# Kernel optimization log

Hardware: AMD Instinct MI355X
Metric: run time of the kernel (lower is better)

The kernel has to match this reference:

```python
import jax, jax.numpy as jnp
import numpy as np


def setup_inputs() -> dict:
    key = jax.random.key(0)
    k1, k2, k3 = jax.random.split(key, 3)
    p = 4096
    target = jax.random.normal(k1, (p, p), dtype=jnp.float32)
    source = jax.random.normal(k2, (p, p), dtype=jnp.float32)
    W_beta = jax.random.uniform(k3, (p, p), dtype=jnp.float32)
    return {"target": target, "source": source, "W_beta": W_beta}


def reference(target, source, W_beta):
    # X = target, Y = source (module-level names in the original).
    # denominator inner loop: sum_i X[i] . X[i] == ||X||_F^2 (scalar),
    # recomputed p^2 times in the original; computed once here.
    s = jnp.sum(target * target)
    W = W_beta.sum(axis=1)                       # [p]
    W2 = W * W                                   # [p]
    scale = W2 / (s * W2 + 1.0)                  # [p]
    G = jnp.matmul(source, target.T)             # [p,p], G[i,j] = Y[i] . X[j]
    W_matrix = scale[:, None] * G                # [p,p]
    primary = jnp.matmul(W_matrix, target) - source
    loss = jnp.sqrt(jnp.sum(jnp.square(jnp.matmul(W_beta, primary))))
    return loss, W_matrix
```

## Files before the change

### kernel.cpp

```cpp
#include <hip/hip_runtime.h>
#include <hip/hip_bf16.h>

#define PDIM 4096
#define PPN ((size_t)PDIM * (size_t)PDIM)

typedef __attribute__((ext_vector_type(8))) short bf16x8;
typedef __attribute__((ext_vector_type(4))) float floatx4;
typedef __attribute__((ext_vector_type(8))) int int8v;

__device__ __forceinline__ void load_lds16(const void* g, void* l) {
  __builtin_amdgcn_global_load_lds(
      (const __attribute__((address_space(1))) void*)g,
      (__attribute__((address_space(3))) void*)l, 16, 0, 0);
}

__device__ __forceinline__ unsigned short bf16bits(float f) {
  __hip_bfloat16 h = __float2bfloat16(f);
  return *(unsigned short*)&h;
}

__device__ __forceinline__ unsigned char fp8byte(float v) {
  return (unsigned char)(__builtin_amdgcn_cvt_pk_fp8_f32(v, v, 0, false) & 0xff);
}
__device__ __forceinline__ unsigned int fp8x4(float a, float b, float c, float d) {
  int v = __builtin_amdgcn_cvt_pk_fp8_f32(a, b, 0, false);
  v = __builtin_amdgcn_cvt_pk_fp8_f32(c, d, v, true);
  return (unsigned int)v;
}

__global__ void sumsq(const float4* __restrict__ x, float* __restrict__ acc) {
  float s = 0.f;
  const size_t n4 = PPN / 4;
  for (size_t i = (size_t)blockIdx.x * 256 + threadIdx.x; i < n4;
       i += (size_t)gridDim.x * 256) {
    const float4 v = x[i];
    s += v.x * v.x + v.y * v.y + v.z * v.z + v.w * v.w;
  }
#pragma unroll
  for (int off = 32; off > 0; off >>= 1) s += __shfl_down(s, off);
  __shared__ float ws[4];
  if ((threadIdx.x & 63) == 0) ws[threadIdx.x >> 6] = s;
  __syncthreads();
  if (threadIdx.x == 0) atomicAdd(acc, ws[0] + ws[1] + ws[2] + ws[3]);
}

__global__ void cast_x(const float* __restrict__ src,
                       __hip_bfloat16* __restrict__ dstN,
                       unsigned char* __restrict__ dstT8) {
  __shared__ float tile[64][65];
  const int bx = blockIdx.x * 64, by = blockIdx.y * 64;
  const int tx = threadIdx.x & 15, ty = threadIdx.x >> 4;
#pragma unroll
  for (int r = 0; r < 4; ++r) {
    const int row = ty + r * 16;
    const float4 v = *(const float4*)&src[(size_t)(by + row) * PDIM + bx + tx * 4];
    tile[row][tx * 4 + 0] = v.x;
    tile[row][tx * 4 + 1] = v.y;
    tile[row][tx * 4 + 2] = v.z;
    tile[row][tx * 4 + 3] = v.w;
    ushort4 o;
    o.x = bf16bits(v.x); o.y = bf16bits(v.y); o.z = bf16bits(v.z); o.w = bf16bits(v.w);
    *(ushort4*)&dstN[(size_t)(by + row) * PDIM + bx + tx * 4] = o;
  }
  __syncthreads();
#pragma unroll
  for (int r = 0; r < 4; ++r) {
    const int i = ty + r * 16;
    *(unsigned int*)&dstT8[(size_t)(bx + i) * PDIM + by + tx * 4] =
        fp8x4(tile[tx * 4 + 0][i], tile[tx * 4 + 1][i],
              tile[tx * 4 + 2][i], tile[tx * 4 + 3][i]);
  }
}

__global__ void cast_y(const float* __restrict__ src,
                       __hip_bfloat16* __restrict__ dstN,
                       __hip_bfloat16* __restrict__ dstT) {
  __shared__ float tile[64][65];
  const int bx = blockIdx.x * 64, by = blockIdx.y * 64;
  const int tx = threadIdx.x & 15, ty = threadIdx.x >> 4;
#pragma unroll
  for (int r = 0; r < 4; ++r) {
    const int row = ty + r * 16;
    const float4 v = *(const float4*)&src[(size_t)(by + row) * PDIM + bx + tx * 4];
    tile[row][tx * 4 + 0] = v.x;
    tile[row][tx * 4 + 1] = v.y;
    tile[row][tx * 4 + 2] = v.z;
    tile[row][tx * 4 + 3] = v.w;
    ushort4 o;
    o.x = bf16bits(v.x); o.y = bf16bits(v.y); o.z = bf16bits(v.z); o.w = bf16bits(v.w);
    *(ushort4*)&dstN[(size_t)(by + row) * PDIM + bx + tx * 4] = o;
  }
  __syncthreads();
#pragma unroll
  for (int r = 0; r < 4; ++r) {
    const int i = ty + r * 16;
    ushort4 o;
    o.x = bf16bits(tile[tx * 4 + 0][i]);
    o.y = bf16bits(tile[tx * 4 + 1][i]);
    o.z = bf16bits(tile[tx * 4 + 2][i]);
    o.w = bf16bits(tile[tx * 4 + 3][i]);
    *(ushort4*)&dstT[(size_t)(bx + i) * PDIM + by + tx * 4] = o;
  }
}

__global__ void cast_wb_rows(const float* __restrict__ Wb,
                             unsigned char* __restrict__ Wb8,
                             const float* __restrict__ sAcc,
                             float* __restrict__ scale) {
  const size_t row = blockIdx.x;
  const float4* src = (const float4*)(Wb + row * PDIM);
  unsigned int* dst = (unsigned int*)(Wb8 + row * PDIM);
  float sum = 0.f;
#pragma unroll
  for (int it = 0; it < 4; ++it) {
    const int j = threadIdx.x + it * 256;
    const float4 v = src[j];
    sum += (v.x + v.y) + (v.z + v.w);
    dst[j] = fp8x4(v.x, v.y, v.z, v.w);
  }
#pragma unroll
  for (int off = 32; off > 0; off >>= 1) sum += __shfl_down(sum, off);
  __shared__ float ws[4];
  if ((threadIdx.x & 63) == 0) ws[threadIdx.x >> 6] = sum;
  __syncthreads();
  if (threadIdx.x == 0) {
    const float W = ws[0] + ws[1] + ws[2] + ws[3];
    const float w2 = W * W;
    scale[row] = w2 / ((*sAcc) * w2 + 1.0f);
  }
}

__device__ __forceinline__ void mfma_quad(floatx4 (&acc)[8][4], int mo, int no,
                                          const bf16x8 (&af)[8],
                                          const bf16x8 (&bf)[4]) {
  __builtin_amdgcn_s_setprio(1);
#pragma unroll
  for (int mi = 0; mi < 4; ++mi)
#pragma unroll
    for (int ni = 0; ni < 2; ++ni)
#pragma unroll
      for (int kk = 0; kk < 2; ++kk)
        acc[mo + mi][no + ni] = __builtin_amdgcn_mfma_f32_16x16x32_bf16(
            af[mi * 2 + kk], bf[ni * 2 + kk], acc[mo + mi][no + ni], 0, 0, 0);
  __builtin_amdgcn_s_setprio(0);
}

__device__ __forceinline__ void read_a(bf16x8 (&dst)[8], const char* base, int slot0) {
#pragma unroll
  for (int mi = 0; mi < 4; ++mi) {
    dst[mi * 2 + 0] = *(const bf16x8*)(base + mi * 2048 + slot0);
    dst[mi * 2 + 1] = *(const bf16x8*)(base + mi * 2048 + (slot0 ^ 64));
  }
}
__device__ __forceinline__ void read_b(bf16x8 (&dst)[4], const char* base, int slot0) {
#pragma unroll
  for (int ni = 0; ni < 2; ++ni) {
    dst[ni * 2 + 0] = *(const bf16x8*)(base + ni * 2048 + slot0);
    dst[ni * 2 + 1] = *(const bf16x8*)(base + ni * 2048 + (slot0 ^ 64));
  }
}

__global__ __launch_bounds__(512, 2)
void gemm_bf16_wm(const __hip_bfloat16* __restrict__ A,
                  const __hip_bfloat16* __restrict__ B,
                  const float* __restrict__ scale,
                  float* __restrict__ outF,
                  unsigned char* __restrict__ Wm8) {
  __shared__ __align__(16) char LDS[131072];

  const int tid = threadIdx.x;
  const int lane = tid & 63;
  const int wave = tid >> 6;
  const int wm = wave >> 2;
  const int wn = wave & 3;

  const int bid = blockIdx.x;
  const int swz = (bid & 7) * 32 + (bid >> 3);
  const int bx = swz & 15;
  const int by = swz >> 4;
  const size_t rowA0 = (size_t)by * 256;
  const size_t rowB0 = (size_t)bx * 256;

  const int srow = tid >> 3;
  const int scol = ((tid & 7) ^ (srow & 7)) << 4;
  const char* pA = (const char*)A + (rowA0 + srow) * 8192 + scol;
  const char* pB = (const char*)B + (rowB0 + srow) * 8192 + scol;
  const int ldsWav = wave * 1024;

  const int fr = lane & 15;
  const int kq = lane >> 4;
  const int slot0 = ((kq ^ (fr & 7)) << 4);
  const int aRowB = (wm * 64 + fr) * 128;
  const int bRowB = (wn * 32 + fr) * 128;

  floatx4 acc[8][4] = {};
  bf16x8 afLo[8], afHi[8], bLo[4], bHi[4];

  {
    char* dA0 = LDS + ldsWav;
    char* dB0 = LDS + 65536 + ldsWav;
    load_lds16(pA, dA0);                         load_lds16(pA + 524288, dA0 + 8192);
    load_lds16(pB, dB0);                         load_lds16(pB + 524288, dB0 + 8192);
    load_lds16(pB + 1048576, dB0 + 16384);       load_lds16(pB + 1572864, dB0 + 24576);
    load_lds16(pA + 1048576, dA0 + 16384);       load_lds16(pA + 1572864, dA0 + 24576);
    char* dA1 = dA0 + 32768;
    char* dB1 = dB0 + 32768;
    load_lds16(pA + 128, dA1);                   load_lds16(pA + 128 + 524288, dA1 + 8192);
    load_lds16(pB + 128, dB1);                   load_lds16(pB + 128 + 524288, dB1 + 8192);
    load_lds16(pB + 128 + 1048576, dB1 + 16384); load_lds16(pB + 128 + 1572864, dB1 + 24576);
    load_lds16(pA + 128 + 1048576, dA1 + 16384); load_lds16(pA + 128 + 1572864, dA1 + 24576);
  }
  asm volatile("s_waitcnt vmcnt(8)" ::: "memory");
  __builtin_amdgcn_s_barrier();
  read_a(afLo, (const char*)LDS + aRowB, slot0);
  read_b(bLo, (const char*)LDS + 65536 + bRowB, slot0);
  asm volatile("s_waitcnt lgkmcnt(0)" ::: "memory");
  __builtin_amdgcn_s_barrier();

  for (int t = 0; t < 64; ++t) {
    const int buf = (t & 1) << 15;
    const int tS = (t + 2) & 63;
    const char* sA = pA + (size_t)tS * 128;
    const char* sB = pB + (size_t)tS * 128;
    char* dA = LDS + buf + ldsWav;
    char* dB = LDS + 65536 + buf + ldsWav;
    const char* aRd  = LDS + buf + aRowB;
    const char* bRd  = LDS + 65536 + buf + bRowB;
    const char* aRdN = LDS + (buf ^ 32768) + aRowB;
    const char* bRdN = LDS + 65536 + (buf ^ 32768) + bRowB;

    load_lds16(sA, dA);
    load_lds16(sA + 524288, dA + 8192);
    mfma_quad(acc, 0, 0, afLo, bLo);
    read_b(bHi, bRd + 16384, slot0);
    __builtin_amdgcn_s_barrier();

    load_lds16(sB, dB);
    load_lds16(sB + 524288, dB + 8192);
    mfma_quad(acc, 0, 2, afLo, bHi);
    read_a(afHi, aRd + 16384, slot0);
    __builtin_amdgcn_s_barrier();

    asm volatile("s_waitcnt vmcnt(10)" ::: "memory");
    load_lds16(sB + 1048576, dB + 16384);
    load_lds16(sB + 1572864, dB + 24576);
    mfma_quad(acc, 4, 2, afHi, bHi);
    read_a(afLo, aRdN, slot0);
    __builtin_amdgcn_s_barrier();

    asm volatile("s_waitcnt vmcnt(6)" ::: "memory");
    load_lds16(sA + 1048576, dA + 16384);
    load_lds16(sA + 1572864, dA + 24576);
    mfma_quad(acc, 4, 0, afHi, bLo);
    read_b(bLo, bRdN, slot0);
    __builtin_amdgcn_s_barrier();
  }

  const int lr = (lane >> 4) << 2;
  const int lc = lane & 15;
#pragma unroll
  for (int mi = 0; mi < 8; ++mi) {
    const size_t rbase = rowA0 + (size_t)(mi >> 2) * 128 + wm * 64 + (mi & 3) * 16 + lr;
#pragma unroll
    for (int r = 0; r < 4; ++r) {
      const size_t row = rbase + r;
      const float sc = scale[row];
#pragma unroll
      for (int ni = 0; ni < 4; ++ni) {
        const size_t col = rowB0 + (size_t)(ni >> 1) * 128 + wn * 32 + (ni & 1) * 16 + lc;
        const float v = sc * acc[mi][ni][r];
        outF[row * PDIM + col] = v;
        Wm8[row * PDIM + col] = fp8byte(v * 131072.f);
      }
    }
  }
}

union f8frag { int8v v; int4 h[2]; };

__device__ __forceinline__ void mfma_quad8(floatx4 (&acc)[8][4], int mo, int no,
                                           const f8frag (&af)[4],
                                           const f8frag (&bf)[2]) {
  __builtin_amdgcn_s_setprio(1);
#pragma unroll
  for (int mi = 0; mi < 4; ++mi)
#pragma unroll
    for (int ni = 0; ni < 2; ++ni)
      acc[mo + mi][no + ni] = __builtin_amdgcn_mfma_scale_f32_16x16x128_f8f6f4(
          af[mi].v, bf[ni].v, acc[mo + mi][no + ni],
          0 , 0 , 0, 0x7F7F7F7F, 0, 0x7F7F7F7F);
  __builtin_amdgcn_s_setprio(0);
}

__device__ __forceinline__ void read_a8(f8frag (&dst)[4], const char* base,
                                        int offLo, int offHi) {
#pragma unroll
  for (int mi = 0; mi < 4; ++mi) {
    dst[mi].h[0] = *(const int4*)(base + mi * 2048 + offLo);
    dst[mi].h[1] = *(const int4*)(base + mi * 2048 + offHi);
  }
}
__device__ __forceinline__ void read_b8(f8frag (&dst)[2], const char* base,
                                        int offLo, int offHi) {
#pragma unroll
  for (int ni = 0; ni < 2; ++ni) {
    dst[ni].h[0] = *(const int4*)(base + ni * 2048 + offLo);
    dst[ni].h[1] = *(const int4*)(base + ni * 2048 + offHi);
  }
}

template <int MODE>
__global__ __launch_bounds__(512, 2)
void gemm_fp8(const unsigned char* __restrict__ A,
              const unsigned char* __restrict__ B,
              const __hip_bfloat16* __restrict__ sub,
              unsigned char* __restrict__ outP,
              float* __restrict__ lossAcc) {
  __shared__ __align__(16) char LDS[131072];

  const int tid = threadIdx.x;
  const int lane = tid & 63;
  const int wave = tid >> 6;
  const int wm = wave >> 2;
  const int wn = wave & 3;

  const int bid = blockIdx.x;
  const int swz = (bid & 7) * 32 + (bid >> 3);
  const int bx = swz & 15;
  const int by = swz >> 4;
  const size_t rowA0 = (size_t)by * 256;
  const size_t rowB0 = (size_t)bx * 256;

  const int srow = tid >> 3;
  const int scol = ((tid & 7) ^ (srow & 7)) << 4;
  const char* pA = (const char*)A + (rowA0 + srow) * 4096 + scol;
  const char* pB = (const char*)B + (rowB0 + srow) * 4096 + scol;
  const int ldsWav = wave * 1024;

  const int fr = lane & 15;
  const int e = fr & 7;
  const int q2 = (lane >> 4) << 1;
  const int offLo = (q2 ^ e) << 4;
  const int offHi = ((q2 + 1) ^ e) << 4;
  const int aRowB = (wm * 64 + fr) * 128;
  const int bRowB = (wn * 32 + fr) * 128;

  floatx4 acc[8][4] = {};
  f8frag afLo[4], afHi[4], bLo[2], bHi[2];

  {
    char* dA0 = LDS + ldsWav;
    char* dB0 = LDS + 65536 + ldsWav;
    load_lds16(pA, dA0);                        load_lds16(pA + 262144, dA0 + 8192);
    load_lds16(pB, dB0);                        load_lds16(pB + 262144, dB0 + 8192);
    load_lds16(pB + 524288, dB0 + 16384);       load_lds16(pB + 786432, dB0 + 24576);
    load_lds16(pA + 524288, dA0 + 16384);       load_lds16(pA + 786432, dA0 + 24576);
    char* dA1 = dA0 + 32768;
    char* dB1 = dB0 + 32768;
    load_lds16(pA + 128, dA1);                  load_lds16(pA + 128 + 262144, dA1 + 8192);
    load_lds16(pB + 128, dB1);                  load_lds16(pB + 128 + 262144, dB1 + 8192);
    load_lds16(pB + 128 + 524288, dB1 + 16384); load_lds16(pB + 128 + 786432, dB1 + 24576);
    load_lds16(pA + 128 + 524288, dA1 + 16384); load_lds16(pA + 128 + 786432, dA1 + 24576);
  }
  asm volatile("s_waitcnt vmcnt(8)" ::: "memory");
  __builtin_amdgcn_s_barrier();
  read_a8(afLo, (const char*)LDS + aRowB, offLo, offHi);
  read_b8(bLo, (const char*)LDS + 65536 + bRowB, offLo, offHi);
  asm volatile("s_waitcnt lgkmcnt(0)" ::: "memory");
  __builtin_amdgcn_s_barrier();

  for (int t = 0; t < 32; ++t) {
    const int buf = (t & 1) << 15;
    const int tS = (t + 2) & 31;
    const char* sA = pA + (size_t)tS * 128;
    const char* sB = pB + (size_t)tS * 128;
    char* dA = LDS + buf + ldsWav;
    char* dB = LDS + 65536 + buf + ldsWav;
    const char* aRd  = LDS + buf + aRowB;
    const char* bRd  = LDS + 65536 + buf + bRowB;
    const char* aRdN = LDS + (buf ^ 32768) + aRowB;
    const char* bRdN = LDS + 65536 + (buf ^ 32768) + bRowB;

    load_lds16(sA, dA);
    load_lds16(sA + 262144, dA + 8192);
    mfma_quad8(acc, 0, 0, afLo, bLo);
    read_b8(bHi, bRd + 16384, offLo, offHi);
    __builtin_amdgcn_s_barrier();

    load_lds16(sB, dB);
    load_lds16(sB + 262144, dB + 8192);
    mfma_quad8(acc, 0, 2, afLo, bHi);
    read_a8(afHi, aRd + 16384, offLo, offHi);
    __builtin_amdgcn_s_barrier();

    asm volatile("s_waitcnt vmcnt(10)" ::: "memory");
    load_lds16(sB + 524288, dB + 16384);
    load_lds16(sB + 786432, dB + 24576);
    mfma_quad8(acc, 4, 2, afHi, bHi);
    read_a8(afLo, aRdN, offLo, offHi);
    __builtin_amdgcn_s_barrier();

    asm volatile("s_waitcnt vmcnt(6)" ::: "memory");
    load_lds16(sA + 524288, dA + 16384);
    load_lds16(sA + 786432, dA + 24576);
    mfma_quad8(acc, 4, 0, afHi, bLo);
    read_b8(bLo, bRdN, offLo, offHi);
    __builtin_amdgcn_s_barrier();
  }

  const int lr = (lane >> 4) << 2;
  const int lc = lane & 15;

  if constexpr (MODE == 2) {
    float tot = 0.f;
#pragma unroll
    for (int mi = 0; mi < 8; ++mi)
#pragma unroll
      for (int ni = 0; ni < 4; ++ni)
#pragma unroll
        for (int r = 0; r < 4; ++r) tot += acc[mi][ni][r] * acc[mi][ni][r];
#pragma unroll
    for (int off = 32; off > 0; off >>= 1) tot += __shfl_down(tot, off);
    __shared__ float ws[8];
    if (lane == 0) ws[wave] = tot;
    __syncthreads();
    if (tid == 0)
      atomicAdd(lossAcc, ws[0] + ws[1] + ws[2] + ws[3] + ws[4] + ws[5] + ws[6] + ws[7]);
  } else {
    constexpr float INV = 1.f / 131072.f;
#pragma unroll
    for (int mi = 0; mi < 8; ++mi) {
      const size_t rbase = rowA0 + (size_t)(mi >> 2) * 128 + wm * 64 + (mi & 3) * 16 + lr;
#pragma unroll
      for (int r = 0; r < 4; ++r) {
        const size_t row = rbase + r;
#pragma unroll
        for (int ni = 0; ni < 4; ++ni) {
          const size_t col = rowB0 + (size_t)(ni >> 1) * 128 + wn * 32 + (ni & 1) * 16 + lc;
          const float v = acc[mi][ni][r] * INV - __bfloat162float(sub[row * PDIM + col]);
          outP[row * PDIM + col] = fp8byte(v);
        }
      }
    }
  }
}

__global__ void finalize(float* __restrict__ out, const float* __restrict__ acc) {
  if (threadIdx.x == 0) out[0] = sqrtf(*acc);
}

extern "C" void kernel_launch(void* const* d_in, const int* in_sizes, int n_in,
                              void* d_out, int out_size, void* d_ws, size_t ws_size,
                              hipStream_t stream) {
  const float* X  = (const float*)d_in[0];
  const float* Y  = (const float*)d_in[1];
  const float* Wb = (const float*)d_in[2];
  float* out = (float*)d_out;

  __hip_bfloat16* Xb   = (__hip_bfloat16*)d_ws;
  __hip_bfloat16* Yb   = Xb + PPN;
  __hip_bfloat16* YbT  = Yb + PPN;
  unsigned char*  XT8  = (unsigned char*)(YbT + PPN);
  unsigned char*  Wm8  = XT8 + PPN;
  unsigned char*  Wb8  = Wm8 + PPN;
  unsigned char*  PT8  = Wb8 + PPN;
  float* scale   = (float*)(PT8 + PPN);
  float* sAcc    = scale + PDIM;
  float* lossAcc = sAcc + 1;

  hipMemsetAsync(sAcc, 0, 2 * sizeof(float), stream);

  sumsq<<<1024, 256, 0, stream>>>((const float4*)X, sAcc);

  dim3 cgrid(PDIM / 64, PDIM / 64);
  cast_x<<<cgrid, 256, 0, stream>>>(X, Xb, XT8);
  cast_y<<<cgrid, 256, 0, stream>>>(Y, Yb, YbT);
  cast_wb_rows<<<PDIM, 256, 0, stream>>>(Wb, Wb8, sAcc, scale);

  gemm_bf16_wm<<<dim3(256), 512, 0, stream>>>(Yb, Xb, scale, out + 1, Wm8);

  gemm_fp8<1><<<dim3(256), 512, 0, stream>>>(XT8, Wm8, YbT, PT8, nullptr);
  gemm_fp8<2><<<dim3(256), 512, 0, stream>>>(PT8, Wb8, nullptr, nullptr, lossAcc);

  finalize<<<1, 1, 0, stream>>>(out, lossAcc);
}
```

Baseline: 520.6 us.

## Fuse sum-of-squares into cast_x and load FP8 GEMM fragments directly from global

The separate sumsq reduction kernel is removed. The Frobenius sum of squares is now accumulated inside cast_x, which already reads X, so one full pass over the input and one launch disappear. The FP8 GEMM no longer stages tiles through LDS with async global-to-LDS copies and barriers. Each wave instead loads its MFMA fragments straight from global memory, prefetching one quarter-step ahead. This drops LDS traffic and barriers, but it gives up sharing data between waves through LDS and exposes global memory latency to the MFMA chain, relying on caches for reuse.

```diff
diff --git a/kernel.cpp b/kernel.cpp
--- a/kernel.cpp
+++ b/kernel.cpp
@@ -28,32 +28,20 @@
   return (unsigned int)v;
 }
 
-__global__ void sumsq(const float4* __restrict__ x, float* __restrict__ acc) {
-  float s = 0.f;
-  const size_t n4 = PPN / 4;
-  for (size_t i = (size_t)blockIdx.x * 256 + threadIdx.x; i < n4;
-       i += (size_t)gridDim.x * 256) {
-    const float4 v = x[i];
-    s += v.x * v.x + v.y * v.y + v.z * v.z + v.w * v.w;
-  }
-#pragma unroll
-  for (int off = 32; off > 0; off >>= 1) s += __shfl_down(s, off);
-  __shared__ float ws[4];
-  if ((threadIdx.x & 63) == 0) ws[threadIdx.x >> 6] = s;
-  __syncthreads();
-  if (threadIdx.x == 0) atomicAdd(acc, ws[0] + ws[1] + ws[2] + ws[3]);
-}
-
 __global__ void cast_x(const float* __restrict__ src,
                        __hip_bfloat16* __restrict__ dstN,
-                       unsigned char* __restrict__ dstT8) {
+                       unsigned char* __restrict__ dstT8,
+                       float* __restrict__ sAcc) {
   __shared__ float tile[64][65];
+  __shared__ float ws[4];
   const int bx = blockIdx.x * 64, by = blockIdx.y * 64;
   const int tx = threadIdx.x & 15, ty = threadIdx.x >> 4;
+  float s = 0.f;
 #pragma unroll
   for (int r = 0; r < 4; ++r) {
     const int row = ty + r * 16;
     const float4 v = *(const float4*)&src[(size_t)(by + row) * PDIM + bx + tx * 4];
+    s += v.x * v.x + v.y * v.y + v.z * v.z + v.w * v.w;
     tile[row][tx * 4 + 0] = v.x;
     tile[row][tx * 4 + 1] = v.y;
     tile[row][tx * 4 + 2] = v.z;
@@ -62,6 +50,9 @@
     o.x = bf16bits(v.x); o.y = bf16bits(v.y); o.z = bf16bits(v.z); o.w = bf16bits(v.w);
     *(ushort4*)&dstN[(size_t)(by + row) * PDIM + bx + tx * 4] = o;
   }
+#pragma unroll
+  for (int off = 32; off > 0; off >>= 1) s += __shfl_down(s, off);
+  if ((threadIdx.x & 63) == 0) ws[threadIdx.x >> 6] = s;
   __syncthreads();
 #pragma unroll
   for (int r = 0; r < 4; ++r) {
@@ -70,6 +61,7 @@
         fp8x4(tile[tx * 4 + 0][i], tile[tx * 4 + 1][i],
               tile[tx * 4 + 2][i], tile[tx * 4 + 3][i]);
   }
+  if (threadIdx.x == 0) atomicAdd(sAcc, ws[0] + ws[1] + ws[2] + ws[3]);
 }
 
 __global__ void cast_y(const float* __restrict__ src,
@@ -292,20 +284,20 @@
   __builtin_amdgcn_s_setprio(0);
 }
 
-__device__ __forceinline__ void read_a8(f8frag (&dst)[4], const char* base,
-                                        int offLo, int offHi) {
+__device__ __forceinline__ void gread_a8(f8frag (&dst)[4],
+                                         const unsigned char* base) {
 #pragma unroll
   for (int mi = 0; mi < 4; ++mi) {
-    dst[mi].h[0] = *(const int4*)(base + mi * 2048 + offLo);
-    dst[mi].h[1] = *(const int4*)(base + mi * 2048 + offHi);
-  }
-}
-__device__ __forceinline__ void read_b8(f8frag (&dst)[2], const char* base,
-                                        int offLo, int offHi) {
+    dst[mi].h[0] = *(const int4*)(base + (size_t)mi * 65536);
+    dst[mi].h[1] = *(const int4*)(base + (size_t)mi * 65536 + 16);
+  }
+}
+__device__ __forceinline__ void gread_b8(f8frag (&dst)[2],
+                                         const unsigned char* base) {
 #pragma unroll
   for (int ni = 0; ni < 2; ++ni) {
-    dst[ni].h[0] = *(const int4*)(base + ni * 2048 + offLo);
-    dst[ni].h[1] = *(const int4*)(base + ni * 2048 + offHi);
+    dst[ni].h[0] = *(const int4*)(base + (size_t)ni * 65536);
+    dst[ni].h[1] = *(const int4*)(base + (size_t)ni * 65536 + 16);
   }
 }
 
@@ -316,8 +308,6 @@
               const __hip_bfloat16* __restrict__ sub,
               unsigned char* __restrict__ outP,
               float* __restrict__ lossAcc) {
-  __shared__ __align__(16) char LDS[131072];
-
   const int tid = threadIdx.x;
   const int lane = tid & 63;
   const int wave = tid >> 6;
@@ -331,81 +321,33 @@
   const size_t rowA0 = (size_t)by * 256;
   const size_t rowB0 = (size_t)bx * 256;
 
-  const int srow = tid >> 3;
-  const int scol = ((tid & 7) ^ (srow & 7)) << 4;
-  const char* pA = (const char*)A + (rowA0 + srow) * 4096 + scol;
-  const char* pB = (const char*)B + (rowB0 + srow) * 4096 + scol;
-  const int ldsWav = wave * 1024;
-
   const int fr = lane & 15;
-  const int e = fr & 7;
   const int q2 = (lane >> 4) << 1;
-  const int offLo = (q2 ^ e) << 4;
-  const int offHi = ((q2 + 1) ^ e) << 4;
-  const int aRowB = (wm * 64 + fr) * 128;
-  const int bRowB = (wn * 32 + fr) * 128;
+
+  const unsigned char* pAlo = A + (rowA0 + wm * 64 + fr) * (size_t)PDIM + q2 * 16;
+  const unsigned char* pAhi = pAlo + (size_t)128 * PDIM;
+  const unsigned char* pBlo = B + (rowB0 + wn * 32 + fr) * (size_t)PDIM + q2 * 16;
+  const unsigned char* pBhi = pBlo + (size_t)128 * PDIM;
 
   floatx4 acc[8][4] = {};
   f8frag afLo[4], afHi[4], bLo[2], bHi[2];
 
-  {
-    char* dA0 = LDS + ldsWav;
-    char* dB0 = LDS + 65536 + ldsWav;
-    load_lds16(pA, dA0);                        load_lds16(pA + 262144, dA0 + 8192);
-    load_lds16(pB, dB0);                        load_lds16(pB + 262144, dB0 + 8192);
-    load_lds16(pB + 524288, dB0 + 16384);       load_lds16(pB + 786432, dB0 + 24576);
-    load_lds16(pA + 524288, dA0 + 16384);       load_lds16(pA + 786432, dA0 + 24576);
-    char* dA1 = dA0 + 32768;
-    char* dB1 = dB0 + 32768;
-    load_lds16(pA + 128, dA1);                  load_lds16(pA + 128 + 262144, dA1 + 8192);
-    load_lds16(pB + 128, dB1);                  load_lds16(pB + 128 + 262144, dB1 + 8192);
-    load_lds16(pB + 128 + 524288, dB1 + 16384); load_lds16(pB + 128 + 786432, dB1 + 24576);
-    load_lds16(pA + 128 + 524288, dA1 + 16384); load_lds16(pA + 128 + 786432, dA1 + 24576);
-  }
-  asm volatile("s_waitcnt vmcnt(8)" ::: "memory");
-  __builtin_amdgcn_s_barrier();
-  read_a8(afLo, (const char*)LDS + aRowB, offLo, offHi);
-  read_b8(bLo, (const char*)LDS + 65536 + bRowB, offLo, offHi);
-  asm volatile("s_waitcnt lgkmcnt(0)" ::: "memory");
-  __builtin_amdgcn_s_barrier();
+  gread_a8(afLo, pAlo);
+  gread_b8(bLo, pBlo);
 
   for (int t = 0; t < 32; ++t) {
-    const int buf = (t & 1) << 15;
-    const int tS = (t + 2) & 31;
-    const char* sA = pA + (size_t)tS * 128;
-    const char* sB = pB + (size_t)tS * 128;
-    char* dA = LDS + buf + ldsWav;
-    char* dB = LDS + 65536 + buf + ldsWav;
-    const char* aRd  = LDS + buf + aRowB;
-    const char* bRd  = LDS + 65536 + buf + bRowB;
-    const char* aRdN = LDS + (buf ^ 32768) + aRowB;
-    const char* bRdN = LDS + 65536 + (buf ^ 32768) + bRowB;
-
-    load_lds16(sA, dA);
-    load_lds16(sA + 262144, dA + 8192);
+    const size_t kt = (size_t)t * 128;
+
     mfma_quad8(acc, 0, 0, afLo, bLo);
-    read_b8(bHi, bRd + 16384, offLo, offHi);
-    __builtin_amdgcn_s_barrier();
-
-    load_lds16(sB, dB);
-    load_lds16(sB + 262144, dB + 8192);
+    gread_b8(bHi, pBhi + kt);
+
     mfma_quad8(acc, 0, 2, afLo, bHi);
-    read_a8(afHi, aRd + 16384, offLo, offHi);
-    __builtin_amdgcn_s_barrier();
-
-    asm volatile("s_waitcnt vmcnt(10)" ::: "memory");
-    load_lds16(sB + 524288, dB + 16384);
-    load_lds16(sB + 786432, dB + 24576);
+    gread_a8(afHi, pAhi + kt);
+
     mfma_quad8(acc, 4, 2, afHi, bHi);
-    read_a8(afLo, aRdN, offLo, offHi);
-    __builtin_amdgcn_s_barrier();
-
-    asm volatile("s_waitcnt vmcnt(6)" ::: "memory");
-    load_lds16(sA + 524288, dA + 16384);
-    load_lds16(sA + 786432, dA + 24576);
+    gread_a8(afLo, pAlo + kt + 128);
     mfma_quad8(acc, 4, 0, afHi, bLo);
-    read_b8(bLo, bRdN, offLo, offHi);
-    __builtin_amdgcn_s_barrier();
+    gread_b8(bLo, pBlo + kt + 128);
   }
 
   const int lr = (lane >> 4) << 2;
@@ -470,10 +412,8 @@
 
   hipMemsetAsync(sAcc, 0, 2 * sizeof(float), stream);
 
-  sumsq<<<1024, 256, 0, stream>>>((const float4*)X, sAcc);
-
   dim3 cgrid(PDIM / 64, PDIM / 64);
-  cast_x<<<cgrid, 256, 0, stream>>>(X, Xb, XT8);
+  cast_x<<<cgrid, 256, 0, stream>>>(X, Xb, XT8, sAcc);
   cast_y<<<cgrid, 256, 0, stream>>>(Y, Yb, YbT);
   cast_wb_rows<<<PDIM, 256, 0, stream>>>(Wb, Wb8, sAcc, scale);
 
```

New measurement: 719.5 us. +38.2%, slower.

## Fuse Frobenius sum-of-squares into cast_x and restructure bf16 GEMM LDS pipeline

Applied to the files above, without the earlier changes.

Removes the separate sumsq kernel by accumulating the squared sum of X inside cast_x, reduced per block and added with one atomic, which avoids a second full read of X and one launch. It also reworks the main loop of the bf16 GEMM: LDS fragment reads are no longer prefetched from the other buffer during the previous step. Each step now reads its own fragments, waits on lgkmcnt, and has extra barriers between the MFMA quads. This lengthens the dependency between LDS reads and MFMAs and may reduce overlap, and the vmcnt(10) wait is dropped, so global-to-LDS ordering depends on the remaining vmcnt(6).

```diff
diff --git a/kernel.cpp b/kernel.cpp
--- a/kernel.cpp
+++ b/kernel.cpp
@@ -28,32 +28,20 @@
   return (unsigned int)v;
 }
 
-__global__ void sumsq(const float4* __restrict__ x, float* __restrict__ acc) {
-  float s = 0.f;
-  const size_t n4 = PPN / 4;
-  for (size_t i = (size_t)blockIdx.x * 256 + threadIdx.x; i < n4;
-       i += (size_t)gridDim.x * 256) {
-    const float4 v = x[i];
-    s += v.x * v.x + v.y * v.y + v.z * v.z + v.w * v.w;
-  }
-#pragma unroll
-  for (int off = 32; off > 0; off >>= 1) s += __shfl_down(s, off);
-  __shared__ float ws[4];
-  if ((threadIdx.x & 63) == 0) ws[threadIdx.x >> 6] = s;
-  __syncthreads();
-  if (threadIdx.x == 0) atomicAdd(acc, ws[0] + ws[1] + ws[2] + ws[3]);
-}
-
 __global__ void cast_x(const float* __restrict__ src,
                        __hip_bfloat16* __restrict__ dstN,
-                       unsigned char* __restrict__ dstT8) {
+                       unsigned char* __restrict__ dstT8,
+                       float* __restrict__ sAcc) {
   __shared__ float tile[64][65];
+  __shared__ float ws[4];
   const int bx = blockIdx.x * 64, by = blockIdx.y * 64;
   const int tx = threadIdx.x & 15, ty = threadIdx.x >> 4;
+  float s = 0.f;
 #pragma unroll
   for (int r = 0; r < 4; ++r) {
     const int row = ty + r * 16;
     const float4 v = *(const float4*)&src[(size_t)(by + row) * PDIM + bx + tx * 4];
+    s += v.x * v.x + v.y * v.y + v.z * v.z + v.w * v.w;
     tile[row][tx * 4 + 0] = v.x;
     tile[row][tx * 4 + 1] = v.y;
     tile[row][tx * 4 + 2] = v.z;
@@ -62,6 +50,9 @@
     o.x = bf16bits(v.x); o.y = bf16bits(v.y); o.z = bf16bits(v.z); o.w = bf16bits(v.w);
     *(ushort4*)&dstN[(size_t)(by + row) * PDIM + bx + tx * 4] = o;
   }
+#pragma unroll
+  for (int off = 32; off > 0; off >>= 1) s += __shfl_down(s, off);
+  if ((threadIdx.x & 63) == 0) ws[threadIdx.x >> 6] = s;
   __syncthreads();
 #pragma unroll
   for (int r = 0; r < 4; ++r) {
@@ -70,6 +61,7 @@
         fp8x4(tile[tx * 4 + 0][i], tile[tx * 4 + 1][i],
               tile[tx * 4 + 2][i], tile[tx * 4 + 3][i]);
   }
+  if (threadIdx.x == 0) atomicAdd(sAcc, ws[0] + ws[1] + ws[2] + ws[3]);
 }
 
 __global__ void cast_y(const float* __restrict__ src,
@@ -212,10 +204,6 @@
   }
   asm volatile("s_waitcnt vmcnt(8)" ::: "memory");
   __builtin_amdgcn_s_barrier();
-  read_a(afLo, (const char*)LDS + aRowB, slot0);
-  read_b(bLo, (const char*)LDS + 65536 + bRowB, slot0);
-  asm volatile("s_waitcnt lgkmcnt(0)" ::: "memory");
-  __builtin_amdgcn_s_barrier();
 
   for (int t = 0; t < 64; ++t) {
     const int buf = (t & 1) << 15;
@@ -224,35 +212,40 @@
     const char* sB = pB + (size_t)tS * 128;
     char* dA = LDS + buf + ldsWav;
     char* dB = LDS + 65536 + buf + ldsWav;
-    const char* aRd  = LDS + buf + aRowB;
-    const char* bRd  = LDS + 65536 + buf + bRowB;
-    const char* aRdN = LDS + (buf ^ 32768) + aRowB;
-    const char* bRdN = LDS + 65536 + (buf ^ 32768) + bRowB;
-
+    const char* aRd = LDS + buf + aRowB;
+    const char* bRd = LDS + 65536 + buf + bRowB;
+
+    read_a(afLo, aRd, slot0);
+    read_b(bLo, bRd, slot0);
+    asm volatile("s_waitcnt lgkmcnt(8)" ::: "memory");
+    __builtin_amdgcn_s_barrier();
+    asm volatile("s_waitcnt lgkmcnt(0)" ::: "memory");
+    mfma_quad(acc, 0, 0, afLo, bLo);
+    __builtin_amdgcn_s_barrier();
+
+    read_b(bHi, bRd + 16384, slot0);
     load_lds16(sA, dA);
     load_lds16(sA + 524288, dA + 8192);
-    mfma_quad(acc, 0, 0, afLo, bLo);
-    read_b(bHi, bRd + 16384, slot0);
-    __builtin_amdgcn_s_barrier();
-
     load_lds16(sB, dB);
     load_lds16(sB + 524288, dB + 8192);
+    __builtin_amdgcn_s_barrier();
+    asm volatile("s_waitcnt lgkmcnt(0)" ::: "memory");
     mfma_quad(acc, 0, 2, afLo, bHi);
+    __builtin_amdgcn_s_barrier();
+
     read_a(afHi, aRd + 16384, slot0);
-    __builtin_amdgcn_s_barrier();
-
-    asm volatile("s_waitcnt vmcnt(10)" ::: "memory");
     load_lds16(sB + 1048576, dB + 16384);
     load_lds16(sB + 1572864, dB + 24576);
+    __builtin_amdgcn_s_barrier();
+    asm volatile("s_waitcnt lgkmcnt(0)" ::: "memory");
     mfma_quad(acc, 4, 2, afHi, bHi);
-    read_a(afLo, aRdN, slot0);
     __builtin_amdgcn_s_barrier();
 
     asm volatile("s_waitcnt vmcnt(6)" ::: "memory");
     load_lds16(sA + 1048576, dA + 16384);
     load_lds16(sA + 1572864, dA + 24576);
+    __builtin_amdgcn_s_barrier();
     mfma_quad(acc, 4, 0, afHi, bLo);
-    read_b(bLo, bRdN, slot0);
     __builtin_amdgcn_s_barrier();
   }
 
@@ -470,10 +463,8 @@
 
   hipMemsetAsync(sAcc, 0, 2 * sizeof(float), stream);
 
-  sumsq<<<1024, 256, 0, stream>>>((const float4*)X, sAcc);
-
   dim3 cgrid(PDIM / 64, PDIM / 64);
-  cast_x<<<cgrid, 256, 0, stream>>>(X, Xb, XT8);
+  cast_x<<<cgrid, 256, 0, stream>>>(X, Xb, XT8, sAcc);
   cast_y<<<cgrid, 256, 0, stream>>>(Y, Yb, YbT);
   cast_wb_rows<<<PDIM, 256, 0, stream>>>(Wb, Wb8, sAcc, scale);
 
```

Result: slower. 535.5 us (+2.9%).
